# Performance work log

Hardware: AMD Instinct MI355X
Metric: run time of the kernel (lower is better)

The kernel has to match this reference:

```python
import math
import jax, jax.numpy as jnp
import numpy as np

B, T, C, H = 2, 1024, 1024, 16
D = C // H
BASE_SCALE = 0.03125
ATTN_ALPHA_INIT, MLP_ALPHA_INIT = 0.05, 0.05


def sinusoidal_embeddings(n, d):
    pos = jnp.arange(n, dtype=jnp.float32)[:, None]
    div = jnp.exp(jnp.arange(0, d, 2, dtype=jnp.float32) * (-math.log(10000.0) / d))
    emb = jnp.zeros((n, d), dtype=jnp.float32)
    emb = emb.at[:, 0::2].set(jnp.sin(pos * div))
    emb = emb.at[:, 1::2].set(jnp.cos(pos * div))
    return emb


def apply_rope(pos, q):
    # pos: (T, D); q: (B, H, T, D). Faithful to source: returns only the rotated-scaled component.
    pos = pos[-q.shape[2]:]
    d = q.shape[-1]
    sin, cos = pos[:, : d // 2], pos[:, d // 2 :]
    q_rot = jnp.stack((-q[..., 1::2], q[..., ::2]), axis=-1)  # (B,H,T,D/2,2)
    sc = jnp.stack((cos, sin), axis=-1)  # (T, D/2, 2)
    return (q_rot * sc).reshape(q.shape)


def justnorm(x):
    return x / jnp.linalg.norm(x, axis=-1, keepdims=True)


def setup_inputs() -> dict:
    key = jax.random.key(0)
    ks = jax.random.split(key, 14)
    w = lambda k, shape: jax.random.normal(k, shape, jnp.float32) * 0.02
    return {
        "h": jax.random.normal(ks[0], (B, T, C), jnp.float32),
        "Wq": w(ks[1], (C, C)),
        "Wk": w(ks[2], (C, C)),
        "Wv": w(ks[3], (C, C)),
        "Wo": w(ks[4], (C, C)),
        "Wfc": w(ks[5], (8 * C, C)),
        "Wproj": w(ks[6], (C, 4 * C)),
        "sqk": BASE_SCALE * jnp.ones(C) + w(ks[7], (C,)) * 0.05,
        "suv": jnp.ones(8 * C) + w(ks[8], (8 * C,)) * 0.05,
        "attn_alpha": BASE_SCALE * jnp.ones(C) + w(ks[9], (C,)) * 0.05,
        "mlp_alpha": BASE_SCALE * jnp.ones(C) + w(ks[10], (C,)) * 0.05,
        "thr_c": 1.6 * jnp.ones(H) + w(ks[11], (H,)) * 0.5,
        "stp": 10.0 * jnp.ones(H),
    }


def reference(h, Wq, Wk, Wv, Wo, Wfc, Wproj, sqk, suv, attn_alpha, mlp_alpha, thr_c, stp):
    softmax_scale = math.sqrt(D)  # nGPT uses sqrt(head_dim) since q,k are unit-normalized

    # --- attention branch (no pre-norm in nGPT mode) ---
    q = (h @ Wq.T).reshape(B, T, H, D).transpose(0, 2, 1, 3)  # (B,H,T,D)
    k = (h @ Wk.T).reshape(B, T, H, D).transpose(0, 2, 1, 3)
    v = (h @ Wv.T).reshape(B, T, H, D).transpose(0, 2, 1, 3)

    pos = sinusoidal_embeddings(T, D)
    q = apply_rope(pos, q)
    k = apply_rope(pos, k)

    sqk_s = (sqk * (1.0 / BASE_SCALE)).reshape(1, H, 1, D)
    q = sqk_s * justnorm(q)
    k = sqk_s * justnorm(k)

    scores = jnp.einsum("bhqd,bhkd->bhqk", q, k) * softmax_scale  # (B,H,T,T)
    causal = jnp.tril(jnp.ones((T, T), dtype=bool))
    w = jax.nn.softmax(jnp.where(causal, scores, -1e9), axis=-1)
    # soft score threshold: per-head sigmoid gate on raw scores, then renormalize
    gate = jax.nn.sigmoid(stp[None, :, None, None] * (scores - thr_c[None, :, None, None]))
    w = w * gate
    w = w / jnp.sum(w, axis=-1, keepdims=True)

    y = jnp.einsum("bhqk,bhkd->bhqd", w, v).transpose(0, 2, 1, 3).reshape(B, T, C)
    h_att = y @ Wo.T

    lr = jnp.abs(attn_alpha * (ATTN_ALPHA_INIT / BASE_SCALE))
    A = justnorm(h)
    Bn = justnorm(h_att)
    h = justnorm(A + lr * (Bn - A))

    # --- MLP branch ---
    uv = h @ Wfc.T  # (B,T,8C)
    uv = (suv * math.sqrt(C)) * uv
    u, vv = jnp.split(uv, 2, axis=-1)
    x_mlp = u * (vv * jax.nn.sigmoid(vv))
    h_mlp = x_mlp @ Wproj.T

    lr2 = jnp.abs(mlp_alpha * (MLP_ALPHA_INIT / BASE_SCALE))
    A = justnorm(h)
    Bn = justnorm(h_mlp)
    h = justnorm(A + lr2 * (Bn - A))
    return h
```

## Files before the change

### kernel.cpp

```cpp
#include <hip/hip_runtime.h>
#include <hip/hip_bf16.h>
#include <math.h>

typedef _Float16 f16x8 __attribute__((ext_vector_type(8)));
typedef float f32x4 __attribute__((ext_vector_type(4)));
typedef float f32x2 __attribute__((ext_vector_type(2)));
typedef unsigned short u16;
typedef unsigned int u32;
typedef u16 u16x4 __attribute__((ext_vector_type(4)));
typedef u16 u16x8 __attribute__((ext_vector_type(8)));

#define DEVI static __device__ __forceinline__
#define LDSS 72
#define MB (1u << 20)

DEVI u16 f2h(float f) {
    _Float16 h = (_Float16)f;
    return __builtin_bit_cast(u16, h);
}
DEVI float h2f(u16 u) {
    return (float)__builtin_bit_cast(_Float16, u);
}
DEVI f32x4 mfma16(f16x8 a, f16x8 b, f32x4 c) {
    return __builtin_amdgcn_mfma_f32_16x16x32_f16(a, b, c, 0, 0, 0);
}
DEVI void gload16(const u16* g, u16* l) {
    __builtin_amdgcn_global_load_lds((const __attribute__((address_space(1))) void*)g,
                                     (__attribute__((address_space(3))) void*)l, 16, 0, 0);
}

DEVI void stage128(const u16* __restrict__ g, size_t row0, int ldg, int k0, u16* lds) {
    int t = threadIdx.x;
    const u16* src = g + (row0 + (size_t)(t >> 3)) * (size_t)ldg + k0 + (t & 7) * 8;
    u16* dst = lds + (t >> 6) * 512;
#pragma unroll
    for (int is = 0; is < 4; is++)
        gload16(src + (size_t)is * 32 * ldg, dst + is * 2048);
}

DEVI void gemm128_core(const u16* __restrict__ A, const u16* __restrict__ B,
                       int ldk, int kbeg, int kend, int m0, int n0,
                       u16* As, u16* Bs, f32x4 acc[4][4]) {
    int lane = threadIdx.x & 63, w = threadIdx.x >> 6;
    int wm = (w >> 1) * 64, wn = (w & 1) * 64;
    int lrow = lane & 15, lg = lane >> 4;
    for (int k0 = kbeg; k0 < kend; k0 += 64) {
        __syncthreads();
        stage128(A, m0, ldk, k0, As);
        stage128(B, n0, ldk, k0, Bs);
        __syncthreads();
#pragma unroll
        for (int ks = 0; ks < 2; ks++) {
            f16x8 af[4], bf[4];
#pragma unroll
            for (int i = 0; i < 4; i++) {
                af[i] = *reinterpret_cast<f16x8*>(&As[(wm + i * 16 + lrow) * 64 + ks * 32 + lg * 8]);
                bf[i] = *reinterpret_cast<f16x8*>(&Bs[(wn + i * 16 + lrow) * 64 + ks * 32 + lg * 8]);
            }
#pragma unroll
            for (int i = 0; i < 4; i++)
#pragma unroll
                for (int j = 0; j < 4; j++)
                    acc[i][j] = mfma16(af[i], bf[j], acc[i][j]);
        }
    }
}

__global__ void cvt_kernel(const float* __restrict__ h, const float* __restrict__ Wq,
                           const float* __restrict__ Wk, const float* __restrict__ Wv,
                           const float* __restrict__ Wo, const float* __restrict__ Wfc,
                           const float* __restrict__ Wproj, u16* __restrict__ dst) {
    int bid = blockIdx.x;
    const float* src;
    size_t doff;
    int sb;
    if (bid < 1024)      { src = h;     sb = 0;    doff = 0; }
    else if (bid < 1536) { src = Wq;    sb = 1024; doff = 2097152; }
    else if (bid < 2048) { src = Wk;    sb = 1536; doff = 3145728; }
    else if (bid < 2560) { src = Wv;    sb = 2048; doff = 4194304; }
    else if (bid < 3072) { src = Wo;    sb = 2560; doff = 5242880; }
    else if (bid < 7168) { src = Wfc;   sb = 3072; doff = 10485760; }
    else                 { src = Wproj; sb = 7168; doff = 6291456; }
    size_t idx = (size_t)(bid - sb) * 2048 + threadIdx.x * 8;
    f32x4 a = *reinterpret_cast<const f32x4*>(src + idx);
    f32x4 b = *reinterpret_cast<const f32x4*>(src + idx + 4);
    u16x8 o;
    o[0] = f2h(a[0]); o[1] = f2h(a[1]); o[2] = f2h(a[2]); o[3] = f2h(a[3]);
    o[4] = f2h(b[0]); o[5] = f2h(b[1]); o[6] = f2h(b[2]); o[7] = f2h(b[3]);
    *reinterpret_cast<u16x8*>(dst + doff + idx) = o;
}

__global__ __launch_bounds__(256, 2) void qkv_h_kernel(
    const u16* __restrict__ hb, const u16* __restrict__ Wqh, const u16* __restrict__ Wkh,
    const u16* __restrict__ Wvh, u16* __restrict__ qb, u16* __restrict__ kb, u16* __restrict__ vb) {
    __shared__ u16 As[128 * 64];
    __shared__ u16 Bs[128 * 64];
    int z = blockIdx.z;
    const u16* W = (z == 0) ? Wqh : (z == 1) ? Wkh : Wvh;
    u16* dst = (z == 0) ? qb : (z == 1) ? kb : vb;
    int m0 = blockIdx.y * 128, n0 = blockIdx.x * 128;
    f32x4 acc[4][4];
    f32x4 zf = {0.f, 0.f, 0.f, 0.f};
#pragma unroll
    for (int i = 0; i < 4; i++)
#pragma unroll
        for (int j = 0; j < 4; j++) acc[i][j] = zf;
    gemm128_core(hb, W, 1024, 0, 1024, m0, n0, As, Bs, acc);
    int lane = threadIdx.x & 63, w = threadIdx.x >> 6;
    int wm = (w >> 1) * 64, wn = (w & 1) * 64;
    int lrow = lane & 15, lg = lane >> 4;
#pragma unroll
    for (int i = 0; i < 4; i++)
#pragma unroll
        for (int j = 0; j < 4; j++)
#pragma unroll
            for (int r = 0; r < 4; r++) {
                int m = m0 + wm + i * 16 + lg * 4 + r;
                int n = n0 + wn + j * 16 + lrow;
                dst[(size_t)m * 1024 + n] = f2h(acc[i][j][r]);
            }
}

__global__ __launch_bounds__(256, 2) void gemm_h_kernel(
    const u16* __restrict__ A, const u16* __restrict__ B, u16* __restrict__ out,
    int ldk, int ksplit, int osplit, int N) {
    __shared__ u16 As[128 * 64];
    __shared__ u16 Bs[128 * 64];
    int z = blockIdx.z;
    int m0 = blockIdx.y * 128, n0 = blockIdx.x * 128;
    f32x4 acc[4][4];
    f32x4 zf = {0.f, 0.f, 0.f, 0.f};
#pragma unroll
    for (int i = 0; i < 4; i++)
#pragma unroll
        for (int j = 0; j < 4; j++) acc[i][j] = zf;
    gemm128_core(A, B, ldk, z * ksplit, (z + 1) * ksplit, m0, n0, As, Bs, acc);
    u16* o = out + (size_t)z * osplit;
    int lane = threadIdx.x & 63, w = threadIdx.x >> 6;
    int wm = (w >> 1) * 64, wn = (w & 1) * 64;
    int lrow = lane & 15, lg = lane >> 4;
#pragma unroll
    for (int i = 0; i < 4; i++)
#pragma unroll
        for (int j = 0; j < 4; j++)
#pragma unroll
            for (int r = 0; r < 4; r++) {
                int m = m0 + wm + i * 16 + lg * 4 + r;
                int n = n0 + wn + j * 16 + lrow;
                o[(size_t)m * N + n] = f2h(acc[i][j][r]);
            }
}

__global__ void qkprep_kernel(u16* __restrict__ qb, u16* __restrict__ kb,
                              const float* __restrict__ sqk) {
    u16* buf = blockIdx.z ? kb : qb;
    int pair = blockIdx.x * 4 + (threadIdx.x >> 6);
    int m = pair >> 4, hh = pair & 15;
    int tt = m & 1023;
    int d = threadIdx.x & 63;
    size_t off = (size_t)m * 1024 + hh * 64 + d;
    float x = h2f(buf[off]);
    float xn = __shfl_xor(x, 1);
    int j = (d & 1) ? ((d - 1) >> 1) : (32 + (d >> 1));
    float dv = exp2f(-(float)(j >> 1) * 0.41524101186092029f);
    float ang = (float)tt * dv;
    float e = (j & 1) ? cosf(ang) : sinf(ang);
    float xr = (d & 1) ? (xn * e) : (-xn * e);
    float ss = xr * xr;
#pragma unroll
    for (int o = 1; o < 64; o <<= 1) ss += __shfl_xor(ss, o);
    float sc = rsqrtf(ss) * sqk[hh * 64 + d] * 32.0f;
    buf[off] = f2h(xr * sc);
}

__global__ __launch_bounds__(128) void attn_kernel(
    const u16* __restrict__ qb, const u16* __restrict__ kb, const u16* __restrict__ vb,
    const float* __restrict__ thr_c, const float* __restrict__ stp,
    float* __restrict__ yp, f32x2* __restrict__ mden) {
    const int T = 1024, C = 1024;
    int qt = 31 - (blockIdx.x >> 1);
    int c = blockIdx.x & 1;
    int bh = blockIdx.y;
    int b = bh >> 4, hh = bh & 15;
    int q0 = qt * 32;
    int nkt = (q0 >> 6) + 1;
    __shared__ u16 Vt[2][64 * LDSS];
    __shared__ u16 Ps[32 * LDSS];
    int t = threadIdx.x;
    int lane = t & 63, w = t >> 6;
    int lrow = lane & 15, lg = lane >> 4, lk = lg * 8;
    int kvp = t & 31, db = t >> 5;

    const u16* qrowp = qb + (size_t)(b * T + q0 + w * 16 + lrow) * C + hh * 64;
    f16x8 qfr[2];
    qfr[0] = *reinterpret_cast<const f16x8*>(qrowp + lk);
    qfr[1] = *reinterpret_cast<const f16x8*>(qrowp + 32 + lk);

    float thr = thr_c[hh], st = stp[hh];
    float stthr = st * thr;
    float mrun = -1e30f, den = 0.f;
    f32x4 yacc[4];
    f32x4 zf = {0.f, 0.f, 0.f, 0.f};
#pragma unroll
    for (int i = 0; i < 4; i++) yacc[i] = zf;
    int qg = q0 + w * 16 + lrow;

    f16x8 kpre[8];
    u16x4 vr[8];
    const u16* kbase0 = kb + (size_t)(b * T + lrow) * C + hh * 64 + lk;
    const u16* vbase0 = vb + (size_t)(b * T + 2 * kvp) * C + hh * 64 + db * 16;

    if (c < nkt) {
        const u16* kbase = kbase0 + (size_t)(c << 6) * C;
        const u16* vsrc = vbase0 + (size_t)(c << 6) * C;
#pragma unroll
        for (int ks = 0; ks < 2; ks++)
#pragma unroll
            for (int f = 0; f < 4; f++)
                kpre[ks * 4 + f] = *reinterpret_cast<const f16x8*>(kbase + (size_t)(f * 16) * C + ks * 32);
#pragma unroll
        for (int dd = 0; dd < 4; dd++) {
            vr[dd * 2] = *reinterpret_cast<const u16x4*>(vsrc + dd * 4);
            vr[dd * 2 + 1] = *reinterpret_cast<const u16x4*>(vsrc + C + dd * 4);
        }
    }

    for (int kt = c; kt < nkt; kt += 2) {
        int kv0 = kt << 6;
        u16* VB = Vt[(kt >> 1) & 1];
#pragma unroll
        for (int dd = 0; dd < 4; dd++)
#pragma unroll
            for (int e = 0; e < 4; e++) {
                u32 v = (u32)vr[dd * 2][e] | ((u32)vr[dd * 2 + 1][e] << 16);
                *reinterpret_cast<u32*>(&VB[(db * 16 + dd * 4 + e) * LDSS + 2 * kvp]) = v;
            }
        f32x4 sacc[4];
#pragma unroll
        for (int f = 0; f < 4; f++) sacc[f] = zf;
#pragma unroll
        for (int ks = 0; ks < 2; ks++)
#pragma unroll
            for (int f = 0; f < 4; f++)
                sacc[f] = mfma16(kpre[ks * 4 + f], qfr[ks], sacc[f]);

        if (kt + 2 < nkt) {
            const u16* kbase = kbase0 + (size_t)((kt + 2) << 6) * C;
            const u16* vsrc = vbase0 + (size_t)((kt + 2) << 6) * C;
#pragma unroll
            for (int ks = 0; ks < 2; ks++)
#pragma unroll
                for (int f = 0; f < 4; f++)
                    kpre[ks * 4 + f] = *reinterpret_cast<const f16x8*>(kbase + (size_t)(f * 16) * C + ks * 32);
#pragma unroll
            for (int dd = 0; dd < 4; dd++) {
                vr[dd * 2] = *reinterpret_cast<const u16x4*>(vsrc + dd * 4);
                vr[dd * 2 + 1] = *reinterpret_cast<const u16x4*>(vsrc + C + dd * 4);
            }
        }

        float svv[16];
        float tmax = -1e30f;
        bool last = (kt == nkt - 1);
#pragma unroll
        for (int f = 0; f < 4; f++)
#pragma unroll
            for (int r = 0; r < 4; r++) {
                float s = sacc[f][r] * 8.0f;
                if (last) {
                    int kvg = kv0 + f * 16 + lg * 4 + r;
                    if (kvg > qg) s = -1e30f;
                }
                svv[f * 4 + r] = s;
                tmax = fmaxf(tmax, s);
            }
        tmax = fmaxf(tmax, __shfl_xor(tmax, 16));
        tmax = fmaxf(tmax, __shfl_xor(tmax, 32));
        float zM = stthr - st * tmax;
        float spM = tmax - __logf(1.0f + __expf(zM));
        float mnew = fmaxf(mrun, spM);
        float alpha = __expf(mrun - mnew);
        float tden = 0.f;
        u16 pu[16];
#pragma unroll
        for (int i = 0; i < 16; i++) {
            float s = svv[i];
            float e2 = __expf(s - mnew);
            float eg = __expf(stthr - st * s);
            float p = e2 * __builtin_amdgcn_rcpf(1.0f + eg);
            u16 ph = f2h(p);
            pu[i] = ph;
            tden += h2f(ph);
        }
        tden += __shfl_xor(tden, 16);
        tden += __shfl_xor(tden, 32);
        den = den * alpha + tden;
        mrun = mnew;

#pragma unroll
        for (int f = 0; f < 4; f++) {
            u16x4 u = {pu[f * 4 + 0], pu[f * 4 + 1], pu[f * 4 + 2], pu[f * 4 + 3]};
            *reinterpret_cast<u16x4*>(&Ps[(w * 16 + lrow) * LDSS + f * 16 + lg * 4]) = u;
        }
        float a4[4];
#pragma unroll
        for (int r = 0; r < 4; r++) a4[r] = __shfl(alpha, lg * 4 + r);
#pragma unroll
        for (int nf = 0; nf < 4; nf++)
#pragma unroll
            for (int r = 0; r < 4; r++) yacc[nf][r] *= a4[r];

        __syncthreads();

#pragma unroll
        for (int ks = 0; ks < 2; ks++) {
            f16x8 pf = *reinterpret_cast<f16x8*>(&Ps[(w * 16 + lrow) * LDSS + ks * 32 + lk]);
#pragma unroll
            for (int nf = 0; nf < 4; nf++) {
                f16x8 vf = *reinterpret_cast<f16x8*>(&VB[(nf * 16 + lrow) * LDSS + ks * 32 + lk]);
                yacc[nf] = mfma16(pf, vf, yacc[nf]);
            }
        }
    }
    float* ypc = yp + (size_t)c * 2097152;
#pragma unroll
    for (int nf = 0; nf < 4; nf++)
#pragma unroll
        for (int r = 0; r < 4; r++) {
            int qrow = q0 + w * 16 + lg * 4 + r;
            ypc[(size_t)(b * T + qrow) * C + hh * 64 + nf * 16 + lrow] = yacc[nf][r];
        }
    if (lg == 0) {
        f32x2 md;
        md[0] = mrun; md[1] = den;
        mden[((size_t)c * 32 + bh) * 1024 + (q0 + w * 16 + lrow)] = md;
    }
}

__global__ void attn_merge_kernel(const float* __restrict__ yp, const f32x2* __restrict__ mden,
                                  u16* __restrict__ y) {
    int row = blockIdx.x;
    int b = row >> 10, tr = row & 1023;
    int t = threadIdx.x;
#pragma unroll
    for (int i = 0; i < 4; i++) {
        int idx = t + 256 * i;
        int hh = idx >> 6;
        f32x2 md0 = mden[((size_t)0 * 32 + b * 16 + hh) * 1024 + tr];
        f32x2 md1 = mden[((size_t)1 * 32 + b * 16 + hh) * 1024 + tr];
        float M = fmaxf(md0[0], md1[0]);
        float w0 = __expf(md0[0] - M), w1 = __expf(md1[0] - M);
        float dn = md0[1] * w0 + md1[1] * w1;
        size_t off = (size_t)row * 1024 + idx;
        float v = (yp[off] * w0 + yp[off + 2097152] * w1) / dn;
        y[off] = f2h(v);
    }
}

__global__ __launch_bounds__(256, 2) void fc_silu_kernel(
    const u16* __restrict__ h1h, const u16* __restrict__ Wfch,
    const float* __restrict__ suv, u16* __restrict__ xmlp) {
    __shared__ u16 As[128 * 64];
    __shared__ u16 Bu[128 * 64];
    __shared__ u16 Bv[128 * 64];
    int m0 = blockIdx.y * 128, n0 = blockIdx.x * 128;
    f32x4 au[4][4], av[4][4];
    f32x4 zf = {0.f, 0.f, 0.f, 0.f};
#pragma unroll
    for (int i = 0; i < 4; i++)
#pragma unroll
        for (int j = 0; j < 4; j++) { au[i][j] = zf; av[i][j] = zf; }
    int lane = threadIdx.x & 63, w = threadIdx.x >> 6;
    int wm = (w >> 1) * 64, wn = (w & 1) * 64;
    int lrow = lane & 15, lg = lane >> 4;
    for (int k0 = 0; k0 < 1024; k0 += 64) {
        __syncthreads();
        stage128(h1h, m0, 1024, k0, As);
        stage128(Wfch, n0, 1024, k0, Bu);
        stage128(Wfch, 4096 + n0, 1024, k0, Bv);
        __syncthreads();
#pragma unroll
        for (int ks = 0; ks < 2; ks++) {
            f16x8 af[4], bu[4], bv[4];
#pragma unroll
            for (int i = 0; i < 4; i++) {
                af[i] = *reinterpret_cast<f16x8*>(&As[(wm + i * 16 + lrow) * 64 + ks * 32 + lg * 8]);
                bu[i] = *reinterpret_cast<f16x8*>(&Bu[(wn + i * 16 + lrow) * 64 + ks * 32 + lg * 8]);
                bv[i] = *reinterpret_cast<f16x8*>(&Bv[(wn + i * 16 + lrow) * 64 + ks * 32 + lg * 8]);
            }
#pragma unroll
            for (int i = 0; i < 4; i++)
#pragma unroll
                for (int j = 0; j < 4; j++) {
                    au[i][j] = mfma16(af[i], bu[j], au[i][j]);
                    av[i][j] = mfma16(af[i], bv[j], av[i][j]);
                }
        }
    }
#pragma unroll
    for (int i = 0; i < 4; i++)
#pragma unroll
        for (int j = 0; j < 4; j++) {
            int n = n0 + wn + j * 16 + lrow;
            float su = suv[n] * 32.0f;
            float sv = suv[4096 + n] * 32.0f;
#pragma unroll
            for (int r = 0; r < 4; r++) {
                int m = m0 + wm + i * 16 + lg * 4 + r;
                float uu = au[i][j][r] * su;
                float vv = av[i][j][r] * sv;
                float sig = 1.0f / (1.0f + __expf(-vv));
                xmlp[(size_t)m * 4096 + n] = f2h(uu * vv * sig);
            }
        }
}

__global__ void normres_kernel(const float* __restrict__ base, const u16* __restrict__ dparts,
                               int nparts, int pstride, const float* __restrict__ alpha,
                               float* __restrict__ outf, u16* __restrict__ outh) {
    int row = blockIdx.x;
    int t = threadIdx.x;
    const float* pb = base + (size_t)row * 1024;
    float xb[4], xd[4];
    float ssb = 0.f, ssd = 0.f;
#pragma unroll
    for (int i = 0; i < 4; i++) {
        size_t off = (size_t)row * 1024 + t + 256 * i;
        xb[i] = pb[t + 256 * i];
        float d = 0.f;
        for (int p = 0; p < nparts; p++) d += h2f(dparts[off + (size_t)p * pstride]);
        xd[i] = d;
        ssb += xb[i] * xb[i];
        ssd += xd[i] * xd[i];
    }
#pragma unroll
    for (int o = 1; o < 64; o <<= 1) { ssb += __shfl_xor(ssb, o); ssd += __shfl_xor(ssd, o); }
    __shared__ float red[8];
    int w = t >> 6;
    if ((t & 63) == 0) { red[w * 2] = ssb; red[w * 2 + 1] = ssd; }
    __syncthreads();
    ssb = red[0] + red[2] + red[4] + red[6];
    ssd = red[1] + red[3] + red[5] + red[7];
    float rb = rsqrtf(ssb), rd = rsqrtf(ssd);
    float c[4];
    float ssc = 0.f;
#pragma unroll
    for (int i = 0; i < 4; i++) {
        float a = xb[i] * rb;
        float bb = xd[i] * rd;
        float lr = fabsf(alpha[t + 256 * i] * 1.6f);
        float cv = a + lr * (bb - a);
        c[i] = cv;
        ssc += cv * cv;
    }
#pragma unroll
    for (int o = 1; o < 64; o <<= 1) ssc += __shfl_xor(ssc, o);
    __syncthreads();
    if ((t & 63) == 0) red[w] = ssc;
    __syncthreads();
    ssc = red[0] + red[1] + red[2] + red[3];
    float rc = rsqrtf(ssc);
#pragma unroll
    for (int i = 0; i < 4; i++) {
        float v = c[i] * rc;
        size_t off = (size_t)row * 1024 + t + 256 * i;
        outf[off] = v;
        if (outh) outh[off] = f2h(v);
    }
}

extern "C" void kernel_launch(void* const* d_in, const int* in_sizes, int n_in,
                              void* d_out, int out_size, void* d_ws, size_t ws_size,
                              hipStream_t stream) {
    const float* h = (const float*)d_in[0];
    const float* Wq = (const float*)d_in[1];
    const float* Wk = (const float*)d_in[2];
    const float* Wv = (const float*)d_in[3];
    const float* Wo = (const float*)d_in[4];
    const float* Wfc = (const float*)d_in[5];
    const float* Wproj = (const float*)d_in[6];
    const float* sqk = (const float*)d_in[7];
    const float* suv = (const float*)d_in[8];
    const float* attn_alpha = (const float*)d_in[9];
    const float* mlp_alpha = (const float*)d_in[10];
    const float* thr_c = (const float*)d_in[11];
    const float* stp = (const float*)d_in[12];

    char* ws = (char*)d_ws;
    u16* f16heap = (u16*)ws;
    u16* hb     = f16heap + 0;
    u16* Wqh    = f16heap + 2097152;
    u16* Wkh    = f16heap + 3145728;
    u16* Wvh    = f16heap + 4194304;
    u16* Woh    = f16heap + 5242880;
    u16* Wprojh = f16heap + 6291456;
    u16* Wfch   = f16heap + 10485760;
    u16* partsP = Wfch;
    u16* qb   = (u16*)(ws + (size_t)36 * MB);
    u16* kb   = (u16*)(ws + (size_t)40 * MB);
    u16* vb   = (u16*)(ws + (size_t)44 * MB);
    u16* y    = (u16*)(ws + (size_t)48 * MB);
    float* yp = (float*)(ws + (size_t)52 * MB);
    f32x2* mden = (f32x2*)(ws + (size_t)68 * MB);
    u16* hattP = (u16*)(ws + (size_t)52 * MB);
    float* h1 = (float*)(ws + (size_t)36 * MB);
    u16* h1h  = (u16*)(ws + (size_t)44 * MB);
    u16* xmlp = (u16*)(ws + (size_t)52 * MB);
    float* out = (float*)d_out;

    cvt_kernel<<<9216, 256, 0, stream>>>(h, Wq, Wk, Wv, Wo, Wfc, Wproj, f16heap);
    qkv_h_kernel<<<dim3(8, 16, 3), 256, 0, stream>>>(hb, Wqh, Wkh, Wvh, qb, kb, vb);
    qkprep_kernel<<<dim3(8192, 1, 2), 256, 0, stream>>>(qb, kb, sqk);
    attn_kernel<<<dim3(64, 32), 128, 0, stream>>>(qb, kb, vb, thr_c, stp, yp, mden);
    attn_merge_kernel<<<2048, 256, 0, stream>>>(yp, mden, y);
    gemm_h_kernel<<<dim3(8, 16, 4), 256, 0, stream>>>(y, Woh, hattP, 1024, 256, 2097152, 1024);
    normres_kernel<<<2048, 256, 0, stream>>>(h, hattP, 4, 2097152, attn_alpha, h1, h1h);
    fc_silu_kernel<<<dim3(32, 16), 256, 0, stream>>>(h1h, Wfch, suv, xmlp);
    gemm_h_kernel<<<dim3(8, 16, 4), 256, 0, stream>>>(xmlp, Wprojh, partsP, 4096, 1024, 2097152, 1024);
    normres_kernel<<<2048, 256, 0, stream>>>(h1, partsP, 4, 2097152, mlp_alpha, out, (u16*)nullptr);
}
```

Before: 205.9 us.

## Split attention KV range four ways and store partial outputs in fp16

The attention kernel now divides each query tile's key/value tiles across four blocks instead of two, doubling the grid to raise occupancy and shorten the longest causal rows. The partial outputs are written as fp16 rather than fp32 to keep the larger partial buffer within the same workspace size, and the merge kernel combines four partials using their max/denominator pairs. This adds more partial traffic and merge work, and unnormalized fp16 partials carry some precision and overflow risk. The partial buffer spans 16MB starting at the 52MB offset, and mden at 68MB now holds four slices.

```diff
diff --git a/kernel.cpp b/kernel.cpp
--- a/kernel.cpp
+++ b/kernel.cpp
@@ -176,10 +176,10 @@
 __global__ __launch_bounds__(128) void attn_kernel(
     const u16* __restrict__ qb, const u16* __restrict__ kb, const u16* __restrict__ vb,
     const float* __restrict__ thr_c, const float* __restrict__ stp,
-    float* __restrict__ yp, f32x2* __restrict__ mden) {
+    u16* __restrict__ yph, f32x2* __restrict__ mden) {
     const int T = 1024, C = 1024;
-    int qt = 31 - (blockIdx.x >> 1);
-    int c = blockIdx.x & 1;
+    int qt = 31 - (blockIdx.x >> 2);
+    int c = blockIdx.x & 3;
     int bh = blockIdx.y;
     int b = bh >> 4, hh = bh & 15;
     int q0 = qt * 32;
@@ -225,9 +225,11 @@
         }
     }
 
-    for (int kt = c; kt < nkt; kt += 2) {
+    int bufsel = 0;
+    for (int kt = c; kt < nkt; kt += 4) {
         int kv0 = kt << 6;
-        u16* VB = Vt[(kt >> 1) & 1];
+        u16* VB = Vt[bufsel];
+        bufsel ^= 1;
 #pragma unroll
         for (int dd = 0; dd < 4; dd++)
 #pragma unroll
@@ -244,9 +246,9 @@
             for (int f = 0; f < 4; f++)
                 sacc[f] = mfma16(kpre[ks * 4 + f], qfr[ks], sacc[f]);
 
-        if (kt + 2 < nkt) {
-            const u16* kbase = kbase0 + (size_t)((kt + 2) << 6) * C;
-            const u16* vsrc = vbase0 + (size_t)((kt + 2) << 6) * C;
+        if (kt + 4 < nkt) {
+            const u16* kbase = kbase0 + (size_t)((kt + 4) << 6) * C;
+            const u16* vsrc = vbase0 + (size_t)((kt + 4) << 6) * C;
 #pragma unroll
             for (int ks = 0; ks < 2; ks++)
 #pragma unroll
@@ -322,13 +324,13 @@
             }
         }
     }
-    float* ypc = yp + (size_t)c * 2097152;
+    u16* ypc = yph + (size_t)c * 2097152;
 #pragma unroll
     for (int nf = 0; nf < 4; nf++)
 #pragma unroll
         for (int r = 0; r < 4; r++) {
             int qrow = q0 + w * 16 + lg * 4 + r;
-            ypc[(size_t)(b * T + qrow) * C + hh * 64 + nf * 16 + lrow] = yacc[nf][r];
+            ypc[(size_t)(b * T + qrow) * C + hh * 64 + nf * 16 + lrow] = f2h(yacc[nf][r]);
         }
     if (lg == 0) {
         f32x2 md;
@@ -337,7 +339,7 @@
     }
 }
 
-__global__ void attn_merge_kernel(const float* __restrict__ yp, const f32x2* __restrict__ mden,
+__global__ void attn_merge_kernel(const u16* __restrict__ yph, const f32x2* __restrict__ mden,
                                   u16* __restrict__ y) {
     int row = blockIdx.x;
     int b = row >> 10, tr = row & 1023;
@@ -346,14 +348,23 @@
     for (int i = 0; i < 4; i++) {
         int idx = t + 256 * i;
         int hh = idx >> 6;
-        f32x2 md0 = mden[((size_t)0 * 32 + b * 16 + hh) * 1024 + tr];
-        f32x2 md1 = mden[((size_t)1 * 32 + b * 16 + hh) * 1024 + tr];
-        float M = fmaxf(md0[0], md1[0]);
-        float w0 = __expf(md0[0] - M), w1 = __expf(md1[0] - M);
-        float dn = md0[1] * w0 + md1[1] * w1;
+        float m[4], d[4];
+        float M = -1e30f;
+#pragma unroll
+        for (int p = 0; p < 4; p++) {
+            f32x2 md = mden[((size_t)p * 32 + b * 16 + hh) * 1024 + tr];
+            m[p] = md[0]; d[p] = md[1];
+            M = fmaxf(M, m[p]);
+        }
         size_t off = (size_t)row * 1024 + idx;
-        float v = (yp[off] * w0 + yp[off + 2097152] * w1) / dn;
-        y[off] = f2h(v);
+        float dn = 0.f, acc = 0.f;
+#pragma unroll
+        for (int p = 0; p < 4; p++) {
+            float wp = __expf(m[p] - M);
+            dn += d[p] * wp;
+            acc += h2f(yph[off + (size_t)p * 2097152]) * wp;
+        }
+        y[off] = f2h(acc / dn);
     }
 }
 
@@ -500,7 +511,7 @@
     u16* kb   = (u16*)(ws + (size_t)40 * MB);
     u16* vb   = (u16*)(ws + (size_t)44 * MB);
     u16* y    = (u16*)(ws + (size_t)48 * MB);
-    float* yp = (float*)(ws + (size_t)52 * MB);
+    u16* yph  = (u16*)(ws + (size_t)52 * MB);
     f32x2* mden = (f32x2*)(ws + (size_t)68 * MB);
     u16* hattP = (u16*)(ws + (size_t)52 * MB);
     float* h1 = (float*)(ws + (size_t)36 * MB);
@@ -511,8 +522,8 @@
     cvt_kernel<<<9216, 256, 0, stream>>>(h, Wq, Wk, Wv, Wo, Wfc, Wproj, f16heap);
     qkv_h_kernel<<<dim3(8, 16, 3), 256, 0, stream>>>(hb, Wqh, Wkh, Wvh, qb, kb, vb);
     qkprep_kernel<<<dim3(8192, 1, 2), 256, 0, stream>>>(qb, kb, sqk);
-    attn_kernel<<<dim3(64, 32), 128, 0, stream>>>(qb, kb, vb, thr_c, stp, yp, mden);
-    attn_merge_kernel<<<2048, 256, 0, stream>>>(yp, mden, y);
+    attn_kernel<<<dim3(128, 32), 128, 0, stream>>>(qb, kb, vb, thr_c, stp, yph, mden);
+    attn_merge_kernel<<<2048, 256, 0, stream>>>(yph, mden, y);
     gemm_h_kernel<<<dim3(8, 16, 4), 256, 0, stream>>>(y, Woh, hattP, 1024, 256, 2097152, 1024);
     normres_kernel<<<2048, 256, 0, stream>>>(h, hattP, 4, 2097152, attn_alpha, h1, h1h);
     fc_silu_kernel<<<dim3(32, 16), 256, 0, stream>>>(h1h, Wfch, suv, xmlp);
```

Measured after the change: 203.5 us (median of 2 runs). Within noise of the previous version (-1.2%).
